# Kernel tuning notes

Measured on AMD Instinct MI355X. Metric: run time of the kernel, lower is better.

The kernel has to match this reference:

```python
import jax, jax.numpy as jnp
import numpy as np

N_NODES = 100000
N_EDGES = 3200000
N_SAMPLES = 8
EPS_CONST = 1e-8


def setup_inputs() -> dict:
    key = jax.random.key(0)
    k1, k2, k3, k4 = jax.random.split(key, 4)
    mu = jax.random.normal(k1, (N_NODES,), dtype=jnp.float32)
    log_sigma = jax.random.normal(k2, (N_NODES,), dtype=jnp.float32)
    eps = jax.random.normal(k3, (N_SAMPLES, N_NODES), dtype=jnp.float32)
    edges = jax.random.randint(k4, (N_EDGES, 2), 0, N_NODES, dtype=jnp.int64)
    return {"mu": mu, "log_sigma": log_sigma, "eps": eps, "edges": edges, "n_samples": N_SAMPLES}


def reference(mu, log_sigma, eps, edges, n_samples):
    # c_samples: [S, N]
    c = mu + jnp.exp(log_sigma) * eps
    ci = c[:, edges[:, 0]]  # [S, E] gather
    cj = c[:, edges[:, 1]]  # [S, E] gather
    p = jax.nn.sigmoid(ci * cj)
    # original: sum over edges of mean over samples
    loglik = jnp.log(p + EPS_CONST).mean(axis=0).sum()
    return loglik
```

## Files before the change

kernel.cpp:

```cpp
#include <hip/hip_runtime.h>
#include <hip/hip_fp16.h>

#define EPS_CONST 1e-8f

__device__ __forceinline__ float logsig_eps(float x) {
    float t = fminf(__expf(-x), 1.0e8f);
    return -__logf(1.0f + t);
}

__global__ void compute_c_h8(const float* __restrict__ mu,
                             const float* __restrict__ ls,
                             const float* __restrict__ eps,
                             __half2* __restrict__ c, int N) {
    int n = blockIdx.x * blockDim.x + threadIdx.x;
    if (n >= N) return;
    float m  = mu[n];
    float sg = __expf(ls[n]);
    float v[8];
#pragma unroll
    for (int s = 0; s < 8; ++s) v[s] = m + sg * eps[(size_t)s * N + n];
    __half2* dst = c + (size_t)n * 4;
#pragma unroll
    for (int s = 0; s < 4; ++s) dst[s] = __floats2half2_rn(v[2 * s], v[2 * s + 1]);
}

__global__ void compute_c_gen(const float* __restrict__ mu,
                              const float* __restrict__ ls,
                              const float* __restrict__ eps,
                              __half* __restrict__ c, int N, int S) {
    int n = blockIdx.x * blockDim.x + threadIdx.x;
    if (n >= N) return;
    float m  = mu[n];
    float sg = __expf(ls[n]);
    for (int s = 0; s < S; ++s) c[(size_t)n * S + s] = __float2half(m + sg * eps[(size_t)s * N + n]);
}

__global__ void detect_and_zero(const unsigned int* __restrict__ raw,
                                int* __restrict__ flag,
                                float* __restrict__ out, int out_size) {
    int lane = threadIdx.x;
    unsigned int acc = 0;
#pragma unroll
    for (int k = 0; k < 4; ++k) acc |= raw[2 * (lane * 4 + k) + 1];
#pragma unroll
    for (int off = 32; off > 0; off >>= 1) acc |= __shfl_down(acc, off, 64);
    if (lane == 0) *flag = (acc == 0u) ? 1 : 0;
    for (int i = lane; i < out_size; i += 64) out[i] = 0.0f;
}

__device__ __forceinline__ float terms8(uint4 A, uint4 B) {
    const __half2* ah = (const __half2*)&A;
    const __half2* bh = (const __half2*)&B;
    float acc = 0.0f;
#pragma unroll
    for (int k = 0; k < 4; ++k) {
        float2 a = __half22float2(ah[k]);
        float2 b = __half22float2(bh[k]);
        acc += logsig_eps(a.x * b.x) + logsig_eps(a.y * b.y);
    }
    return acc;
}

__global__ void edge_loglik_s8(const void* __restrict__ edges_raw,
                               const uint4* __restrict__ c,
                               const int* __restrict__ flag,
                               float* __restrict__ out,
                               long long E, float inv_s) {
    long long tid    = (long long)blockIdx.x * blockDim.x + threadIdx.x;
    long long stride = (long long)gridDim.x * blockDim.x;
    float acc = 0.0f;
    bool is64 = (*flag != 0);

    if (!is64) {
        const int4* ep = (const int4*)edges_raw;
        long long P = E >> 1;
        for (long long p = tid; p < P; p += stride) {
            int4 ee = ep[p];
            uint4 a = c[ee.x];
            uint4 b = c[ee.y];
            uint4 d = c[ee.z];
            uint4 f = c[ee.w];
            acc += terms8(a, b) + terms8(d, f);
        }
        if ((E & 1) && tid == 0) {
            const int2* el = (const int2*)edges_raw;
            int2 ij = el[E - 1];
            acc += terms8(c[ij.x], c[ij.y]);
        }
    } else {
        const longlong2* ep = (const longlong2*)edges_raw;
        for (long long e = tid; e < E; e += stride) {
            longlong2 ij = ep[e];
            acc += terms8(c[ij.x], c[ij.y]);
        }
    }

#pragma unroll
    for (int off = 32; off > 0; off >>= 1) acc += __shfl_down(acc, off, 64);
    __shared__ float wsum[8];
    int lane = threadIdx.x & 63;
    int wid  = threadIdx.x >> 6;
    if (lane == 0) wsum[wid] = acc;
    __syncthreads();
    if (threadIdx.x == 0) {
        float s = 0.0f;
        int nw = blockDim.x >> 6;
        for (int w = 0; w < nw; ++w) s += wsum[w];
        atomicAdd(out, s * inv_s);
    }
}

__global__ void edge_loglik_gen(const void* __restrict__ edges_raw,
                                const __half* __restrict__ c,
                                const int* __restrict__ flag,
                                float* __restrict__ out,
                                long long E, int S, float inv_s) {
    long long tid    = (long long)blockIdx.x * blockDim.x + threadIdx.x;
    long long stride = (long long)gridDim.x * blockDim.x;
    float acc = 0.0f;
    bool is64 = (*flag != 0);
    for (long long e = tid; e < E; e += stride) {
        long long i, j;
        if (is64) {
            const long long* ed = (const long long*)edges_raw;
            i = ed[2 * e]; j = ed[2 * e + 1];
        } else {
            const int* ed = (const int*)edges_raw;
            i = ed[2 * e]; j = ed[2 * e + 1];
        }
        for (int s = 0; s < S; ++s)
            acc += logsig_eps(__half2float(c[i * S + s]) * __half2float(c[j * S + s]));
    }
#pragma unroll
    for (int off = 32; off > 0; off >>= 1) acc += __shfl_down(acc, off, 64);
    __shared__ float wsum[8];
    int lane = threadIdx.x & 63;
    int wid  = threadIdx.x >> 6;
    if (lane == 0) wsum[wid] = acc;
    __syncthreads();
    if (threadIdx.x == 0) {
        float s = 0.0f;
        int nw = blockDim.x >> 6;
        for (int w = 0; w < nw; ++w) s += wsum[w];
        atomicAdd(out, s * inv_s);
    }
}

extern "C" void kernel_launch(void* const* d_in, const int* in_sizes, int n_in,
                              void* d_out, int out_size, void* d_ws, size_t ws_size,
                              hipStream_t stream) {
    const float* mu    = (const float*)d_in[0];
    const float* ls    = (const float*)d_in[1];
    const float* eps   = (const float*)d_in[2];
    const void*  edges = d_in[3];

    int       N = in_sizes[0];
    int       S = in_sizes[2] / N;
    long long E = (long long)in_sizes[3] / 2;

    __half* c   = (__half*)d_ws;
    int*   flag = (int*)((char*)d_ws + (size_t)N * S * sizeof(__half) + 256);
    float* out  = (float*)d_out;

    detect_and_zero<<<1, 64, 0, stream>>>((const unsigned int*)edges, flag, out, out_size);

    int cblocks = (N + 255) / 256;
    if (S == 8) {
        compute_c_h8<<<cblocks, 256, 0, stream>>>(mu, ls, eps, (__half2*)c, N);
        edge_loglik_s8<<<2048, 256, 0, stream>>>(edges, (const uint4*)c, flag, out, E, 1.0f / (float)S);
    } else {
        compute_c_gen<<<cblocks, 256, 0, stream>>>(mu, ls, eps, c, N, S);
        edge_loglik_gen<<<2048, 256, 0, stream>>>(edges, c, flag, out, E, S, 1.0f / (float)S);
    }
}
```

Baseline: 54.50 us.

## Fuse detect kernel into compute_c, use product-of-logs, fp16 multiply, and unroll edge loop

Folds the edge-dtype detection and output zeroing into an extra block of the compute_c kernel, removing one kernel launch. The per-edge math now multiplies in half2 precision, then replaces eight logs with two by accumulating products (1+t_i) through FMAs before taking the log. The edge loop handles two strided pairs per iteration to expose more memory-level parallelism, and launch bounds are added. Products of up to four factors each clamped at 1e8 can overflow float, and the half-precision multiply loses accuracy, so numerics may drift from the reference.

```diff
diff --git a/kernel.cpp b/kernel.cpp
--- a/kernel.cpp
+++ b/kernel.cpp
@@ -1,17 +1,27 @@
 #include <hip/hip_runtime.h>
 #include <hip/hip_fp16.h>
 
-#define EPS_CONST 1e-8f
-
-__device__ __forceinline__ float logsig_eps(float x) {
-    float t = fminf(__expf(-x), 1.0e8f);
-    return -__logf(1.0f + t);
-}
 
 __global__ void compute_c_h8(const float* __restrict__ mu,
                              const float* __restrict__ ls,
                              const float* __restrict__ eps,
-                             __half2* __restrict__ c, int N) {
+                             __half2* __restrict__ c, int N,
+                             const unsigned int* __restrict__ raw_edges,
+                             int* __restrict__ flag,
+                             float* __restrict__ out, int out_size) {
+    if (blockIdx.x == gridDim.x - 1) {
+        int lane = threadIdx.x;
+        if (lane < 64) {
+            unsigned int acc = 0;
+#pragma unroll
+            for (int k = 0; k < 4; ++k) acc |= raw_edges[2 * (lane * 4 + k) + 1];
+#pragma unroll
+            for (int off = 32; off > 0; off >>= 1) acc |= __shfl_down(acc, off, 64);
+            if (lane == 0) *flag = (acc == 0u) ? 1 : 0;
+        }
+        for (int i = threadIdx.x; i < out_size; i += blockDim.x) out[i] = 0.0f;
+        return;
+    }
     int n = blockIdx.x * blockDim.x + threadIdx.x;
     if (n >= N) return;
     float m  = mu[n];
@@ -27,7 +37,23 @@
 __global__ void compute_c_gen(const float* __restrict__ mu,
                               const float* __restrict__ ls,
                               const float* __restrict__ eps,
-                              __half* __restrict__ c, int N, int S) {
+                              __half* __restrict__ c, int N, int S,
+                              const unsigned int* __restrict__ raw_edges,
+                              int* __restrict__ flag,
+                              float* __restrict__ out, int out_size) {
+    if (blockIdx.x == gridDim.x - 1) {
+        int lane = threadIdx.x;
+        if (lane < 64) {
+            unsigned int acc = 0;
+#pragma unroll
+            for (int k = 0; k < 4; ++k) acc |= raw_edges[2 * (lane * 4 + k) + 1];
+#pragma unroll
+            for (int off = 32; off > 0; off >>= 1) acc |= __shfl_down(acc, off, 64);
+            if (lane == 0) *flag = (acc == 0u) ? 1 : 0;
+        }
+        for (int i = threadIdx.x; i < out_size; i += blockDim.x) out[i] = 0.0f;
+        return;
+    }
     int n = blockIdx.x * blockDim.x + threadIdx.x;
     if (n >= N) return;
     float m  = mu[n];
@@ -35,37 +61,34 @@
     for (int s = 0; s < S; ++s) c[(size_t)n * S + s] = __float2half(m + sg * eps[(size_t)s * N + n]);
 }
 
-__global__ void detect_and_zero(const unsigned int* __restrict__ raw,
-                                int* __restrict__ flag,
-                                float* __restrict__ out, int out_size) {
-    int lane = threadIdx.x;
-    unsigned int acc = 0;
-#pragma unroll
-    for (int k = 0; k < 4; ++k) acc |= raw[2 * (lane * 4 + k) + 1];
-#pragma unroll
-    for (int off = 32; off > 0; off >>= 1) acc |= __shfl_down(acc, off, 64);
-    if (lane == 0) *flag = (acc == 0u) ? 1 : 0;
-    for (int i = lane; i < out_size; i += 64) out[i] = 0.0f;
-}
-
-__device__ __forceinline__ float terms8(uint4 A, uint4 B) {
+__device__ __forceinline__ float edge_term(uint4 A, uint4 B) {
     const __half2* ah = (const __half2*)&A;
     const __half2* bh = (const __half2*)&B;
-    float acc = 0.0f;
+    float t[8];
 #pragma unroll
     for (int k = 0; k < 4; ++k) {
-        float2 a = __half22float2(ah[k]);
-        float2 b = __half22float2(bh[k]);
-        acc += logsig_eps(a.x * b.x) + logsig_eps(a.y * b.y);
-    }
-    return acc;
-}
-
-__global__ void edge_loglik_s8(const void* __restrict__ edges_raw,
-                               const uint4* __restrict__ c,
-                               const int* __restrict__ flag,
-                               float* __restrict__ out,
-                               long long E, float inv_s) {
+        __half2 xh = __hmul2(ah[k], bh[k]);
+        float2 xf = __half22float2(xh);
+        t[2 * k]     = fminf(__expf(-xf.x), 1.0e8f);
+        t[2 * k + 1] = fminf(__expf(-xf.y), 1.0e8f);
+    }
+    float p0 = 1.0f + t[0];
+    p0 = __builtin_fmaf(p0, t[1], p0);
+    p0 = __builtin_fmaf(p0, t[2], p0);
+    p0 = __builtin_fmaf(p0, t[3], p0);
+    float p1 = 1.0f + t[4];
+    p1 = __builtin_fmaf(p1, t[5], p1);
+    p1 = __builtin_fmaf(p1, t[6], p1);
+    p1 = __builtin_fmaf(p1, t[7], p1);
+    return __logf(p0) + __logf(p1);
+}
+
+__global__ void __launch_bounds__(256, 8)
+edge_loglik_s8(const void* __restrict__ edges_raw,
+               const uint4* __restrict__ c,
+               const int* __restrict__ flag,
+               float* __restrict__ out,
+               long long E, float inv_s) {
     long long tid    = (long long)blockIdx.x * blockDim.x + threadIdx.x;
     long long stride = (long long)gridDim.x * blockDim.x;
     float acc = 0.0f;
@@ -74,24 +97,27 @@
     if (!is64) {
         const int4* ep = (const int4*)edges_raw;
         long long P = E >> 1;
-        for (long long p = tid; p < P; p += stride) {
-            int4 ee = ep[p];
-            uint4 a = c[ee.x];
-            uint4 b = c[ee.y];
-            uint4 d = c[ee.z];
-            uint4 f = c[ee.w];
-            acc += terms8(a, b) + terms8(d, f);
+        for (long long q = tid; q < P; q += 2 * stride) {
+            long long q1 = q + stride;
+            bool has1 = q1 < P;
+            int4 e0 = ep[q];
+            int4 e1 = has1 ? ep[q1] : e0;
+            uint4 a0 = c[e0.x], b0 = c[e0.y], d0 = c[e0.z], f0 = c[e0.w];
+            uint4 a1 = c[e1.x], b1 = c[e1.y], d1 = c[e1.z], f1 = c[e1.w];
+            float s = edge_term(a0, b0) + edge_term(d0, f0);
+            if (has1) s += edge_term(a1, b1) + edge_term(d1, f1);
+            acc += s;
         }
         if ((E & 1) && tid == 0) {
             const int2* el = (const int2*)edges_raw;
             int2 ij = el[E - 1];
-            acc += terms8(c[ij.x], c[ij.y]);
+            acc += edge_term(c[ij.x], c[ij.y]);
         }
     } else {
         const longlong2* ep = (const longlong2*)edges_raw;
         for (long long e = tid; e < E; e += stride) {
             longlong2 ij = ep[e];
-            acc += terms8(c[ij.x], c[ij.y]);
+            acc += edge_term(c[ij.x], c[ij.y]);
         }
     }
 
@@ -106,7 +132,7 @@
         float s = 0.0f;
         int nw = blockDim.x >> 6;
         for (int w = 0; w < nw; ++w) s += wsum[w];
-        atomicAdd(out, s * inv_s);
+        atomicAdd(out, -s * inv_s);
     }
 }
 
@@ -128,8 +154,10 @@
             const int* ed = (const int*)edges_raw;
             i = ed[2 * e]; j = ed[2 * e + 1];
         }
-        for (int s = 0; s < S; ++s)
-            acc += logsig_eps(__half2float(c[i * S + s]) * __half2float(c[j * S + s]));
+        for (int s = 0; s < S; ++s) {
+            float x = __half2float(c[i * S + s]) * __half2float(c[j * S + s]);
+            acc += __logf(1.0f + fminf(__expf(-x), 1.0e8f));
+        }
     }
 #pragma unroll
     for (int off = 32; off > 0; off >>= 1) acc += __shfl_down(acc, off, 64);
@@ -142,7 +170,7 @@
         float s = 0.0f;
         int nw = blockDim.x >> 6;
         for (int w = 0; w < nw; ++w) s += wsum[w];
-        atomicAdd(out, s * inv_s);
+        atomicAdd(out, -s * inv_s);
     }
 }
 
@@ -162,14 +190,14 @@
     int*   flag = (int*)((char*)d_ws + (size_t)N * S * sizeof(__half) + 256);
     float* out  = (float*)d_out;
 
-    detect_and_zero<<<1, 64, 0, stream>>>((const unsigned int*)edges, flag, out, out_size);
-
-    int cblocks = (N + 255) / 256;
+    int cblocks = (N + 255) / 256 + 1;
     if (S == 8) {
-        compute_c_h8<<<cblocks, 256, 0, stream>>>(mu, ls, eps, (__half2*)c, N);
+        compute_c_h8<<<cblocks, 256, 0, stream>>>(mu, ls, eps, (__half2*)c, N,
+                                                  (const unsigned int*)edges, flag, out, out_size);
         edge_loglik_s8<<<2048, 256, 0, stream>>>(edges, (const uint4*)c, flag, out, E, 1.0f / (float)S);
     } else {
-        compute_c_gen<<<cblocks, 256, 0, stream>>>(mu, ls, eps, c, N, S);
+        compute_c_gen<<<cblocks, 256, 0, stream>>>(mu, ls, eps, c, N, S,
+                                                   (const unsigned int*)edges, flag, out, out_size);
         edge_loglik_gen<<<2048, 256, 0, stream>>>(edges, c, flag, out, E, S, 1.0f / (float)S);
     }
 }
```

Measured after the change: 48.06 us. 1.13x faster.
